# Performance work log

Hardware: AMD Instinct MI355X
Metric: run time of the kernel (lower is better)

Reference implementation:

```python
import jax, jax.numpy as jnp
import numpy as np

N = 40000
K = 16
NUM_CLASSES = 8
BN_EPS = 1e-5


def _mlp(h, W1, b1, g, bt, m, v, W2, b2):
    # Linear -> ReLU -> BatchNorm1d (eval mode, running stats) -> Linear
    h = jax.nn.relu(h @ W1 + b1)
    h = (h - m) / jnp.sqrt(v + BN_EPS) * g + bt
    return h @ W2 + b2


def _normals(pos, nbr):
    # cross product of first two neighbor offsets, normalized; fallback [0,0,1]
    v1 = pos[nbr[:, 0]] - pos
    v2 = pos[nbr[:, 1]] - pos
    n = jnp.cross(v1, v2)
    nrm = jnp.linalg.norm(n, axis=-1, keepdims=True)
    unit = n / jnp.maximum(nrm, 1e-12)
    up = jnp.array([0.0, 0.0, 1.0], dtype=pos.dtype)
    return jnp.where(nrm > 0, unit, up)


def _pointnet_conv(x, pos, nbr_all, W1, b1, g, bt, m, v, W2, b2):
    # PyG PointNetConv: msg = local_nn(cat[x_j, pos_j - pos_i]); max-aggregate
    xj = x[nbr_all]                        # [N, K+1, F]
    rel = pos[nbr_all] - pos[:, None, :]   # [N, K+1, 3]
    msg = _mlp(jnp.concatenate([xj, rel], axis=-1), W1, b1, g, bt, m, v, W2, b2)
    return msg.max(axis=1)


def setup_inputs():
    key = jax.random.key(0)
    ks = jax.random.split(key, 32)

    def lin_w(k, fi, fo):
        return (jax.random.normal(k, (fi, fo), jnp.float32) / np.sqrt(fi)).astype(jnp.float32)

    def vec(k, d, scale=0.01):
        return scale * jax.random.normal(k, (d,), jnp.float32)

    return {
        "pos": jax.random.normal(ks[0], (N, 3), jnp.float32),
        "neighbor_idx": jax.random.randint(ks[1], (N, K), 0, N),
        # local_features: Linear(9,64), ReLU, BN(64), Linear(64,128)
        "W1": lin_w(ks[2], 9, 64), "b1": vec(ks[3], 64),
        "g1": 1.0 + 0.1 * jax.random.normal(ks[4], (64,), jnp.float32),
        "bt1": vec(ks[5], 64), "m1": vec(ks[6], 64, 0.1),
        "v1": jax.random.uniform(ks[7], (64,), jnp.float32, minval=0.5, maxval=1.5),
        "W2": lin_w(ks[8], 64, 128), "b2": vec(ks[9], 128),
        # roof_features: Linear(131,128), ReLU, BN(128), Linear(128,256)
        "W3": lin_w(ks[10], 131, 128), "b3": vec(ks[11], 128),
        "g2": 1.0 + 0.1 * jax.random.normal(ks[12], (128,), jnp.float32),
        "bt2": vec(ks[13], 128), "m2": vec(ks[14], 128, 0.1),
        "v2": jax.random.uniform(ks[15], (128,), jnp.float32, minval=0.5, maxval=1.5),
        "W4": lin_w(ks[16], 128, 256), "b4": vec(ks[17], 256),
        # classifier: Linear(256, num_classes)
        "Wc": lin_w(ks[18], 256, NUM_CLASSES), "bc": vec(ks[19], NUM_CLASSES),
    }


def reference(pos, neighbor_idx, W1, b1, g1, bt1, m1, v1, W2, b2,
              W3, b3, g2, bt2, m2, v2, W4, b4, Wc, bc):
    x = pos  # data.x is used as both features and coordinates
    normals = _normals(pos, neighbor_idx)
    x = jnp.concatenate([x, normals], axis=1)  # [N, 6]
    # PointNetConv adds self-loops by default
    self_idx = jnp.arange(pos.shape[0], dtype=neighbor_idx.dtype)[:, None]
    nbr_all = jnp.concatenate([neighbor_idx, self_idx], axis=1)  # [N, K+1]
    x = jax.nn.relu(_pointnet_conv(x, pos, nbr_all, W1, b1, g1, bt1, m1, v1, W2, b2))
    x = jax.nn.relu(_pointnet_conv(x, pos, nbr_all, W3, b3, g2, bt2, m2, v2, W4, b4))
    logits = x @ Wc + bc
    return jax.nn.log_softmax(logits, axis=-1)
```

## Files before the change

kernel.cpp:

```cpp
#include <hip/hip_runtime.h>
#include <math.h>

#define NPTS 40000
#define KNBR 16
#define BN_EPS 1e-5f

typedef __attribute__((ext_vector_type(8))) short v8s;
typedef __attribute__((ext_vector_type(4))) float f32x4;

__device__ __forceinline__ unsigned short f2bf(float f) {
    union { float f; unsigned int u; } c; c.f = f;
    unsigned int u = c.u + 0x7fffu + ((c.u >> 16) & 1u);
    return (unsigned short)(u >> 16);
}
__device__ __forceinline__ float bflo(unsigned int u) {
    union { unsigned int u; float f; } c; c.u = u << 16; return c.f;
}
__device__ __forceinline__ float bfhi(unsigned int u) {
    union { unsigned int u; float f; } c; c.u = u & 0xffff0000u; return c.f;
}

__global__ __launch_bounds__(256, 4)
void k1_b1(const float* __restrict__ pos, const int* __restrict__ nbr,
           const float* __restrict__ W1, const float* __restrict__ b1,
           unsigned short* __restrict__ B1) {
    int p = blockIdx.x * 4 + (threadIdx.x >> 6);
    int k = threadIdx.x & 63;
    float px = pos[p * 3 + 0], py = pos[p * 3 + 1], pz = pos[p * 3 + 2];
    int n0 = nbr[p * KNBR + 0], n1 = nbr[p * KNBR + 1];
    float ax = pos[n0 * 3 + 0] - px, ay = pos[n0 * 3 + 1] - py, az = pos[n0 * 3 + 2] - pz;
    float bx = pos[n1 * 3 + 0] - px, by = pos[n1 * 3 + 1] - py, bz = pos[n1 * 3 + 2] - pz;
    float cx = ay * bz - az * by;
    float cy = az * bx - ax * bz;
    float cz = ax * by - ay * bx;
    float nrm = sqrtf(cx * cx + cy * cy + cz * cz);
    float inv = 1.0f / fmaxf(nrm, 1e-12f);
    float ux, uy, uz;
    if (nrm > 0.0f) { ux = cx * inv; uy = cy * inv; uz = cz * inv; }
    else            { ux = 0.0f;     uy = 0.0f;     uz = 1.0f;     }
    float acc = b1[k];
    acc = fmaf(px, W1[0 * 64 + k], acc);
    acc = fmaf(py, W1[1 * 64 + k], acc);
    acc = fmaf(pz, W1[2 * 64 + k], acc);
    acc = fmaf(ux, W1[3 * 64 + k], acc);
    acc = fmaf(uy, W1[4 * 64 + k], acc);
    acc = fmaf(uz, W1[5 * 64 + k], acc);
    B1[p * 64 + k] = f2bf(acc);
}

#define PTS2 32
__global__ __launch_bounds__(256, 2)
void k2_conv1_mfma(const float* __restrict__ pos, const int* __restrict__ nbr,
                   const unsigned short* __restrict__ B1, const float* __restrict__ W1,
                   const float* __restrict__ g1, const float* __restrict__ bt1,
                   const float* __restrict__ m1, const float* __restrict__ v1,
                   const float* __restrict__ W2, const float* __restrict__ b2,
                   const float* __restrict__ W3, const float* __restrict__ b3,
                   unsigned short* __restrict__ A2) {
    __shared__ __align__(16) unsigned char Tl[2][16 * 128];
    __shared__ __align__(16) unsigned char Hl[32 * 256];
    __shared__ float Ssf1[32 * 128];

    const int tid  = threadIdx.x;
    const int wv   = tid >> 6;
    const int lane = tid & 63;
    const int lgrp = lane >> 4;
    const int lmod = lane & 15;

    v8s Bf2[2][2];
    float b2c[2];
#pragma unroll
    for (int nt = 0; nt < 2; ++nt) {
        const int col = wv * 32 + nt * 16 + lmod;
        b2c[nt] = b2[col];
#pragma unroll
        for (int kt = 0; kt < 2; ++kt)
#pragma unroll
            for (int j = 0; j < 8; ++j)
                Bf2[nt][kt][j] = (short)f2bf(W2[(kt * 32 + lgrp * 8 + j) * 128 + col]);
    }
    const int ch0 = (lane & 31) * 2;
    const int rsub = lane >> 5;
    const float w6a = W1[6 * 64 + ch0],     w7a = W1[7 * 64 + ch0],     w8a = W1[8 * 64 + ch0];
    const float w6b = W1[6 * 64 + ch0 + 1], w7b = W1[7 * 64 + ch0 + 1], w8b = W1[8 * 64 + ch0 + 1];
    const float s1a = g1[ch0] * rsqrtf(v1[ch0] + BN_EPS);
    const float o1a = bt1[ch0] - m1[ch0] * s1a;
    const float s1b = g1[ch0 + 1] * rsqrtf(v1[ch0 + 1] + BN_EPS);
    const float o1b = bt1[ch0 + 1] - m1[ch0 + 1] * s1b;

    const int base = blockIdx.x * PTS2;

#pragma unroll
    for (int pr = 0; pr < 16; ++pr) {
        const int pl = pr * 2 + rsub;
        const unsigned int a = *(const unsigned int*)&B1[(size_t)(base + pl) * 64 + ch0];
        const float ta = fmaf(fmaxf(bflo(a), 0.f), s1a, o1a);
        const float tb = fmaf(fmaxf(bfhi(a), 0.f), s1b, o1b);
        const unsigned int w = (unsigned int)f2bf(ta) | ((unsigned int)f2bf(tb) << 16);
        const int row = pl & 15;
        int byte = row * 128 + ch0 * 2;
        byte ^= (row & 7) << 4;
        *(unsigned int*)(Tl[pl >> 4] + byte) = w;
    }
    __syncthreads();
    {
        f32x4 accS[2][2];
#pragma unroll
        for (int hf = 0; hf < 2; ++hf)
#pragma unroll
            for (int nt = 0; nt < 2; ++nt) accS[hf][nt] = f32x4{0.f, 0.f, 0.f, 0.f};
#pragma unroll
        for (int hf = 0; hf < 2; ++hf)
#pragma unroll
            for (int kt = 0; kt < 2; ++kt) {
                int b0 = lmod * 128 + kt * 64 + lgrp * 16;
                b0 ^= (lmod & 7) << 4;
                const v8s a0 = *(const v8s*)(Tl[hf] + b0);
#pragma unroll
                for (int nt = 0; nt < 2; ++nt)
                    accS[hf][nt] = __builtin_amdgcn_mfma_f32_16x16x32_bf16(a0, Bf2[nt][kt], accS[hf][nt], 0, 0, 0);
            }
#pragma unroll
        for (int hf = 0; hf < 2; ++hf)
#pragma unroll
            for (int nt = 0; nt < 2; ++nt)
#pragma unroll
                for (int reg = 0; reg < 4; ++reg)
                    Ssf1[(hf * 16 + lgrp * 4 + reg) * 128 + wv * 32 + nt * 16 + lmod] = accS[hf][nt][reg];
    }
    __syncthreads();

    {
        const int i = base;
        const float cx = pos[i * 3 + 0], cy = pos[i * 3 + 1], cz = pos[i * 3 + 2];
#pragma unroll
        for (int it = 0; it < 2; ++it) {
            const int m = it * 8 + wv * 2 + rsub;
            const int idx = nbr[i * KNBR + m];
            const unsigned int a = *(const unsigned int*)&B1[(size_t)idx * 64 + ch0];
            const float rx = pos[idx * 3 + 0] - cx;
            const float ry = pos[idx * 3 + 1] - cy;
            const float rz = pos[idx * 3 + 2] - cz;
            float pa = bflo(a);
            pa = fmaf(rx, w6a, pa); pa = fmaf(ry, w7a, pa); pa = fmaf(rz, w8a, pa);
            float pb = bfhi(a);
            pb = fmaf(rx, w6b, pb); pb = fmaf(ry, w7b, pb); pb = fmaf(rz, w8b, pb);
            const float ta = fmaf(fmaxf(pa, 0.f), s1a, o1a);
            const float tb = fmaf(fmaxf(pb, 0.f), s1b, o1b);
            const unsigned int w = (unsigned int)f2bf(ta) | ((unsigned int)f2bf(tb) << 16);
            int byte = m * 128 + ch0 * 2;
            byte ^= (m & 7) << 4;
            *(unsigned int*)(Tl[0] + byte) = w;
        }
    }
    unsigned int aCur[2], aNxt[2];
    float pCx[2], pCy[2], pCz[2], pNx[2], pNy[2], pNz[2];
#pragma unroll
    for (int it = 0; it < 2; ++it) { aCur[it] = 0u; aNxt[it] = 0u; pCx[it]=pCy[it]=pCz[it]=pNx[it]=pNy[it]=pNz[it]=0.f; }
    {
        const int in_ = base + 1;
#pragma unroll
        for (int it = 0; it < 2; ++it) {
            const int m = it * 8 + wv * 2 + rsub;
            const int idx = nbr[in_ * KNBR + m];
            aCur[it] = *(const unsigned int*)&B1[(size_t)idx * 64 + ch0];
            pCx[it] = pos[idx * 3 + 0]; pCy[it] = pos[idx * 3 + 1]; pCz[it] = pos[idx * 3 + 2];
        }
    }
    __syncthreads();

    for (int p = 0; p < PTS2; ++p) {
        const int buf = p & 1;
        if (p < PTS2 - 2) {
            const int in2 = base + p + 2;
#pragma unroll
            for (int it = 0; it < 2; ++it) {
                const int m = it * 8 + wv * 2 + rsub;
                const int idx = nbr[in2 * KNBR + m];
                aNxt[it] = *(const unsigned int*)&B1[(size_t)idx * 64 + ch0];
                pNx[it] = pos[idx * 3 + 0]; pNy[it] = pos[idx * 3 + 1]; pNz[it] = pos[idx * 3 + 2];
            }
        }
        f32x4 acc0[2];
        acc0[0] = f32x4{0.f, 0.f, 0.f, 0.f};
        acc0[1] = f32x4{0.f, 0.f, 0.f, 0.f};
#pragma unroll
        for (int kt = 0; kt < 2; ++kt) {
            int b0 = lmod * 128 + kt * 64 + lgrp * 16;
            b0 ^= (lmod & 7) << 4;
            const v8s a0 = *(const v8s*)(Tl[buf] + b0);
#pragma unroll
            for (int nt = 0; nt < 2; ++nt)
                acc0[nt] = __builtin_amdgcn_mfma_f32_16x16x32_bf16(a0, Bf2[nt][kt], acc0[nt], 0, 0, 0);
        }
#pragma unroll
        for (int nt = 0; nt < 2; ++nt) {
            float mv = fmaxf(fmaxf(acc0[nt][0], acc0[nt][1]),
                             fmaxf(acc0[nt][2], acc0[nt][3]));
            mv = fmaxf(mv, __shfl_xor(mv, 16));
            mv = fmaxf(mv, __shfl_xor(mv, 32));
            const float ss = Ssf1[p * 128 + wv * 32 + nt * 16 + lmod];
            const float h = fmaxf(fmaxf(mv, ss) + b2c[nt], 0.f);
            if (lgrp == 0) {
                int hb = p * 256 + (wv * 32 + nt * 16 + lmod) * 2;
                hb ^= (p & 7) << 4;
                *(unsigned short*)(Hl + hb) = f2bf(h);
            }
        }
        if (p < PTS2 - 1) {
            const int in_ = base + p + 1;
            const float ccx = pos[in_ * 3 + 0], ccy = pos[in_ * 3 + 1], ccz = pos[in_ * 3 + 2];
#pragma unroll
            for (int it = 0; it < 2; ++it) {
                const int m = it * 8 + wv * 2 + rsub;
                const float rx = pCx[it] - ccx, ry = pCy[it] - ccy, rz = pCz[it] - ccz;
                float pa = bflo(aCur[it]);
                pa = fmaf(rx, w6a, pa); pa = fmaf(ry, w7a, pa); pa = fmaf(rz, w8a, pa);
                float pb = bfhi(aCur[it]);
                pb = fmaf(rx, w6b, pb); pb = fmaf(ry, w7b, pb); pb = fmaf(rz, w8b, pb);
                const float ta = fmaf(fmaxf(pa, 0.f), s1a, o1a);
                const float tb = fmaf(fmaxf(pb, 0.f), s1b, o1b);
                const unsigned int w = (unsigned int)f2bf(ta) | ((unsigned int)f2bf(tb) << 16);
                int byte = m * 128 + ch0 * 2;
                byte ^= (m & 7) << 4;
                *(unsigned int*)(Tl[buf ^ 1] + byte) = w;
            }
        }
        __syncthreads();
#pragma unroll
        for (int it = 0; it < 2; ++it) {
            aCur[it] = aNxt[it];
            pCx[it] = pNx[it]; pCy[it] = pNy[it]; pCz[it] = pNz[it];
        }
    }

    v8s Wf3[2][4];
    float b3c[2];
#pragma unroll
    for (int nt = 0; nt < 2; ++nt) {
        const int col = wv * 32 + nt * 16 + lmod;
        b3c[nt] = b3[col];
#pragma unroll
        for (int kt = 0; kt < 4; ++kt)
#pragma unroll
            for (int j = 0; j < 8; ++j)
                Wf3[nt][kt][j] = (short)f2bf(W3[(kt * 32 + lgrp * 8 + j) * 128 + col]);
    }
    f32x4 accA[2][2];
#pragma unroll
    for (int mt = 0; mt < 2; ++mt)
#pragma unroll
        for (int nt = 0; nt < 2; ++nt) accA[mt][nt] = f32x4{0.f, 0.f, 0.f, 0.f};
#pragma unroll
    for (int kt = 0; kt < 4; ++kt) {
#pragma unroll
        for (int mt = 0; mt < 2; ++mt) {
            int ba = (mt * 16 + lmod) * 256 + kt * 64 + lgrp * 16;
            ba ^= (lmod & 7) << 4;
            const v8s aH = *(const v8s*)(Hl + ba);
#pragma unroll
            for (int nt = 0; nt < 2; ++nt)
                accA[mt][nt] = __builtin_amdgcn_mfma_f32_16x16x32_bf16(aH, Wf3[nt][kt], accA[mt][nt], 0, 0, 0);
        }
    }
#pragma unroll
    for (int mt = 0; mt < 2; ++mt)
#pragma unroll
        for (int nt = 0; nt < 2; ++nt)
#pragma unroll
            for (int reg = 0; reg < 4; ++reg) {
                const int row = base + mt * 16 + lgrp * 4 + reg;
                const int col = wv * 32 + nt * 16 + lmod;
                A2[(size_t)row * 128 + col] = f2bf(accA[mt][nt][reg] + b3c[nt]);
            }
}

#define PTS4 32
__global__ __launch_bounds__(256, 2)
void k4_conv2_mfma(const float* __restrict__ pos, const int* __restrict__ nbr,
                   const unsigned short* __restrict__ A2, const float* __restrict__ W3,
                   const float* __restrict__ g2, const float* __restrict__ bt2,
                   const float* __restrict__ m2, const float* __restrict__ v2,
                   const float* __restrict__ W4, const float* __restrict__ b4,
                   const float* __restrict__ Wc,
                   float* __restrict__ Z) {
    __shared__ __align__(16) unsigned char Tl[2][16 * 256];
    __shared__ float Ssf[32 * 256];

    const int tid  = threadIdx.x;
    const int wv   = tid >> 6;
    const int lane = tid & 63;
    const int lgrp = lane >> 4;
    const int lmod = lane & 15;

    v8s Bf[4][4];
#pragma unroll
    for (int nt = 0; nt < 4; ++nt) {
        const int col = wv * 64 + nt * 16 + lmod;
#pragma unroll
        for (int kt = 0; kt < 4; ++kt)
#pragma unroll
            for (int j = 0; j < 8; ++j)
                Bf[nt][kt][j] = (short)f2bf(W4[(kt * 32 + lgrp * 8 + j) * 256 + col]);
    }
    float wcls[4][8]; float b4c[4];
#pragma unroll
    for (int nt = 0; nt < 4; ++nt) {
        const int col = wv * 64 + nt * 16 + lmod;
        b4c[nt] = b4[col];
#pragma unroll
        for (int c = 0; c < 8; ++c) wcls[nt][c] = Wc[col * 8 + c];
    }
    const int ch0 = lane * 2;
    const float bw0a = W3[128 * 128 + ch0],     bw1a = W3[129 * 128 + ch0],     bw2a = W3[130 * 128 + ch0];
    const float bw0b = W3[128 * 128 + ch0 + 1], bw1b = W3[129 * 128 + ch0 + 1], bw2b = W3[130 * 128 + ch0 + 1];
    const float sa = g2[ch0] * rsqrtf(v2[ch0] + BN_EPS);
    const float oa = bt2[ch0] - m2[ch0] * sa;
    const float sb = g2[ch0 + 1] * rsqrtf(v2[ch0 + 1] + BN_EPS);
    const float ob = bt2[ch0 + 1] - m2[ch0 + 1] * sb;

    const int base = blockIdx.x * PTS4;

#pragma unroll
    for (int pl = 0; pl < 16; ++pl) {
        {
            const unsigned int a = *(const unsigned int*)&A2[(size_t)(base + pl) * 128 + ch0];
            const float ta = fmaf(fmaxf(bflo(a), 0.f), sa, oa);
            const float tb = fmaf(fmaxf(bfhi(a), 0.f), sb, ob);
            const unsigned int w = (unsigned int)f2bf(ta) | ((unsigned int)f2bf(tb) << 16);
            int byte = pl * 256 + ch0 * 2;
            byte ^= (pl & 7) << 4;
            *(unsigned int*)(Tl[0] + byte) = w;
        }
        {
            const unsigned int a = *(const unsigned int*)&A2[(size_t)(base + 16 + pl) * 128 + ch0];
            const float ta = fmaf(fmaxf(bflo(a), 0.f), sa, oa);
            const float tb = fmaf(fmaxf(bfhi(a), 0.f), sb, ob);
            const unsigned int w = (unsigned int)f2bf(ta) | ((unsigned int)f2bf(tb) << 16);
            int byte = pl * 256 + ch0 * 2;
            byte ^= (pl & 7) << 4;
            *(unsigned int*)(Tl[1] + byte) = w;
        }
    }
    __syncthreads();
    {
        f32x4 accS[2][4];
#pragma unroll
        for (int hf = 0; hf < 2; ++hf)
#pragma unroll
            for (int nt = 0; nt < 4; ++nt) accS[hf][nt] = f32x4{0.f, 0.f, 0.f, 0.f};
#pragma unroll
        for (int hf = 0; hf < 2; ++hf)
#pragma unroll
            for (int kt = 0; kt < 4; ++kt) {
                int b0 = lmod * 256 + kt * 64 + lgrp * 16;
                b0 ^= (lmod & 7) << 4;
                const v8s a0 = *(const v8s*)(Tl[hf] + b0);
#pragma unroll
                for (int nt = 0; nt < 4; ++nt)
                    accS[hf][nt] = __builtin_amdgcn_mfma_f32_16x16x32_bf16(a0, Bf[nt][kt], accS[hf][nt], 0, 0, 0);
            }
#pragma unroll
        for (int hf = 0; hf < 2; ++hf)
#pragma unroll
            for (int nt = 0; nt < 4; ++nt)
#pragma unroll
                for (int reg = 0; reg < 4; ++reg)
                    Ssf[(hf * 16 + lgrp * 4 + reg) * 256 + wv * 64 + nt * 16 + lmod] = accS[hf][nt][reg];
    }
    __syncthreads();

    {
        const int i = base;
        const float cx = pos[i * 3 + 0], cy = pos[i * 3 + 1], cz = pos[i * 3 + 2];
#pragma unroll
        for (int it = 0; it < 4; ++it) {
            const int m = it * 4 + wv;
            const int idx = nbr[i * KNBR + m];
            const unsigned int a = *(const unsigned int*)&A2[(size_t)idx * 128 + ch0];
            const float rx = pos[idx * 3 + 0] - cx;
            const float ry = pos[idx * 3 + 1] - cy;
            const float rz = pos[idx * 3 + 2] - cz;
            float pa = bflo(a);
            pa = fmaf(rx, bw0a, pa); pa = fmaf(ry, bw1a, pa); pa = fmaf(rz, bw2a, pa);
            float pb = bfhi(a);
            pb = fmaf(rx, bw0b, pb); pb = fmaf(ry, bw1b, pb); pb = fmaf(rz, bw2b, pb);
            const float ta = fmaf(fmaxf(pa, 0.f), sa, oa);
            const float tb = fmaf(fmaxf(pb, 0.f), sb, ob);
            const unsigned int w = (unsigned int)f2bf(ta) | ((unsigned int)f2bf(tb) << 16);
            int byte = m * 256 + ch0 * 2;
            byte ^= (m & 7) << 4;
            *(unsigned int*)(Tl[0] + byte) = w;
        }
    }
    unsigned int aCur[4], aNxt[4];
    float pCx[4], pCy[4], pCz[4], pNx[4], pNy[4], pNz[4];
#pragma unroll
    for (int it = 0; it < 4; ++it) { aCur[it] = 0u; aNxt[it] = 0u; pCx[it]=pCy[it]=pCz[it]=pNx[it]=pNy[it]=pNz[it]=0.f; }
    {
        const int in_ = base + 1;
#pragma unroll
        for (int it = 0; it < 4; ++it) {
            const int m = it * 4 + wv;
            const int idx = nbr[in_ * KNBR + m];
            aCur[it] = *(const unsigned int*)&A2[(size_t)idx * 128 + ch0];
            pCx[it] = pos[idx * 3 + 0]; pCy[it] = pos[idx * 3 + 1]; pCz[it] = pos[idx * 3 + 2];
        }
    }
    __syncthreads();

    for (int p = 0; p < PTS4; ++p) {
        const int buf = p & 1;
        if (p < PTS4 - 2) {
            const int in2 = base + p + 2;
#pragma unroll
            for (int it = 0; it < 4; ++it) {
                const int m = it * 4 + wv;
                const int idx = nbr[in2 * KNBR + m];
                aNxt[it] = *(const unsigned int*)&A2[(size_t)idx * 128 + ch0];
                pNx[it] = pos[idx * 3 + 0]; pNy[it] = pos[idx * 3 + 1]; pNz[it] = pos[idx * 3 + 2];
            }
        }
        f32x4 acc0[4];
#pragma unroll
        for (int nt = 0; nt < 4; ++nt) acc0[nt] = f32x4{0.f, 0.f, 0.f, 0.f};
#pragma unroll
        for (int kt = 0; kt < 4; ++kt) {
            int b0 = lmod * 256 + kt * 64 + lgrp * 16;
            b0 ^= (lmod & 7) << 4;
            const v8s a0 = *(const v8s*)(Tl[buf] + b0);
#pragma unroll
            for (int nt = 0; nt < 4; ++nt)
                acc0[nt] = __builtin_amdgcn_mfma_f32_16x16x32_bf16(a0, Bf[nt][kt], acc0[nt], 0, 0, 0);
        }
        float part[8];
#pragma unroll
        for (int c = 0; c < 8; ++c) part[c] = 0.f;
#pragma unroll
        for (int nt = 0; nt < 4; ++nt) {
            float mv = fmaxf(fmaxf(acc0[nt][0], acc0[nt][1]),
                             fmaxf(acc0[nt][2], acc0[nt][3]));
            mv = fmaxf(mv, __shfl_xor(mv, 16));
            mv = fmaxf(mv, __shfl_xor(mv, 32));
            const float ss = Ssf[p * 256 + wv * 64 + nt * 16 + lmod];
            const float h = fmaxf(fmaxf(mv, ss) + b4c[nt], 0.f);
#pragma unroll
            for (int c = 0; c < 8; ++c) part[c] = fmaf(h, wcls[nt][c], part[c]);
        }
#pragma unroll
        for (int c = 0; c < 8; ++c) {
            part[c] += __shfl_xor(part[c], 1);
            part[c] += __shfl_xor(part[c], 2);
            part[c] += __shfl_xor(part[c], 4);
            part[c] += __shfl_xor(part[c], 8);
        }
        if (lane == 0) {
#pragma unroll
            for (int c = 0; c < 8; ++c)
                Z[(size_t)(base + p) * 32 + wv * 8 + c] = part[c];
        }
        if (p < PTS4 - 1) {
            const int in_ = base + p + 1;
            const float ccx = pos[in_ * 3 + 0], ccy = pos[in_ * 3 + 1], ccz = pos[in_ * 3 + 2];
#pragma unroll
            for (int it = 0; it < 4; ++it) {
                const int m = it * 4 + wv;
                const float rx = pCx[it] - ccx, ry = pCy[it] - ccy, rz = pCz[it] - ccz;
                float pa = bflo(aCur[it]);
                pa = fmaf(rx, bw0a, pa); pa = fmaf(ry, bw1a, pa); pa = fmaf(rz, bw2a, pa);
                float pb = bfhi(aCur[it]);
                pb = fmaf(rx, bw0b, pb); pb = fmaf(ry, bw1b, pb); pb = fmaf(rz, bw2b, pb);
                const float ta = fmaf(fmaxf(pa, 0.f), sa, oa);
                const float tb = fmaf(fmaxf(pb, 0.f), sb, ob);
                const unsigned int w = (unsigned int)f2bf(ta) | ((unsigned int)f2bf(tb) << 16);
                int byte = m * 256 + ch0 * 2;
                byte ^= (m & 7) << 4;
                *(unsigned int*)(Tl[buf ^ 1] + byte) = w;
            }
        }
        __syncthreads();
#pragma unroll
        for (int it = 0; it < 4; ++it) {
            aCur[it] = aNxt[it];
            pCx[it] = pNx[it]; pCy[it] = pNy[it]; pCz[it] = pNz[it];
        }
    }
}

__global__ __launch_bounds__(256, 4)
void k5_softmax(const float* __restrict__ Z, const float* __restrict__ bc,
                float* __restrict__ out) {
    const int i = blockIdx.x * 256 + threadIdx.x;
    if (i >= NPTS) return;
    float z[8];
#pragma unroll
    for (int c = 0; c < 8; ++c) z[c] = bc[c];
#pragma unroll
    for (int w = 0; w < 4; ++w) {
        const float4 a = *(const float4*)&Z[(size_t)i * 32 + w * 8 + 0];
        const float4 b = *(const float4*)&Z[(size_t)i * 32 + w * 8 + 4];
        z[0] += a.x; z[1] += a.y; z[2] += a.z; z[3] += a.w;
        z[4] += b.x; z[5] += b.y; z[6] += b.z; z[7] += b.w;
    }
    float mz = z[0];
#pragma unroll
    for (int c = 1; c < 8; ++c) mz = fmaxf(mz, z[c]);
    float se = 0.f;
#pragma unroll
    for (int c = 0; c < 8; ++c) se += expf(z[c] - mz);
    const float lse = mz + logf(se);
#pragma unroll
    for (int c = 0; c < 8; ++c) out[(size_t)i * 8 + c] = z[c] - lse;
}

extern "C" void kernel_launch(void* const* d_in, const int* in_sizes, int n_in,
                              void* d_out, int out_size, void* d_ws, size_t ws_size,
                              hipStream_t stream) {
    const float* pos = (const float*)d_in[0];
    const int*   nbr = (const int*)d_in[1];
    const float* W1  = (const float*)d_in[2];
    const float* b1  = (const float*)d_in[3];
    const float* g1  = (const float*)d_in[4];
    const float* bt1 = (const float*)d_in[5];
    const float* m1  = (const float*)d_in[6];
    const float* v1  = (const float*)d_in[7];
    const float* W2  = (const float*)d_in[8];
    const float* b2  = (const float*)d_in[9];
    const float* W3  = (const float*)d_in[10];
    const float* b3  = (const float*)d_in[11];
    const float* g2  = (const float*)d_in[12];
    const float* bt2 = (const float*)d_in[13];
    const float* m2  = (const float*)d_in[14];
    const float* v2  = (const float*)d_in[15];
    const float* W4  = (const float*)d_in[16];
    const float* b4  = (const float*)d_in[17];
    const float* Wc  = (const float*)d_in[18];
    const float* bc  = (const float*)d_in[19];
    float* out = (float*)d_out;

    unsigned short* B1 = (unsigned short*)d_ws;
    unsigned short* A2 = B1 + (size_t)NPTS * 64;
    float* Z = (float*)(A2 + (size_t)NPTS * 128);

    k1_b1<<<NPTS / 4, 256, 0, stream>>>(pos, nbr, W1, b1, B1);
    k2_conv1_mfma<<<NPTS / PTS2, 256, 0, stream>>>(pos, nbr, B1, W1, g1, bt1, m1, v1,
                                                   W2, b2, W3, b3, A2);
    k4_conv2_mfma<<<NPTS / PTS4, 256, 0, stream>>>(pos, nbr, A2, W3, g2, bt2, m2, v2,
                                                   W4, b4, Wc, Z);
    k5_softmax<<<(NPTS + 255) / 256, 256, 0, stream>>>(Z, bc, out);
}
```

Before: 320.9 us.

## Process four points per pipeline step with one wave per point gather

Both conv kernels now handle a group of four points per loop iteration, with each wave gathering all 16 neighbors of one point using a wave-uniform (readfirstlane) index. This replaces the old one-point-per-iteration loop, so there are a quarter as many barriers and each gather load is larger. The self-term scratch is stored as bf16 instead of fp32 to fit the larger 64-row tiles in LDS, and in conv2 the classifier weights are read from memory per use instead of being held in registers. In exchange, the kernels use more LDS and more registers for prefetch, and the bf16 self-term adds some rounding error.

Measured after the change: 319.8 us. Within noise of the previous version (-0.3%).

```diff
diff --git a/kernel.cpp b/kernel.cpp
--- a/kernel.cpp
+++ b/kernel.cpp
@@ -18,6 +18,9 @@
 }
 __device__ __forceinline__ float bfhi(unsigned int u) {
     union { unsigned int u; float f; } c; c.u = u & 0xffff0000u; return c.f;
+}
+__device__ __forceinline__ float bf2f(unsigned short u) {
+    union { unsigned int u; float f; } c; c.u = ((unsigned int)u) << 16; return c.f;
 }
 
 __global__ __launch_bounds__(256, 4)
@@ -49,6 +52,7 @@
 }
 
 #define PTS2 32
+#define NG2 8
 __global__ __launch_bounds__(256, 2)
 void k2_conv1_mfma(const float* __restrict__ pos, const int* __restrict__ nbr,
                    const unsigned short* __restrict__ B1, const float* __restrict__ W1,
@@ -57,9 +61,9 @@
                    const float* __restrict__ W2, const float* __restrict__ b2,
                    const float* __restrict__ W3, const float* __restrict__ b3,
                    unsigned short* __restrict__ A2) {
-    __shared__ __align__(16) unsigned char Tl[2][16 * 128];
+    __shared__ __align__(16) unsigned char Tl[2][64 * 128];
     __shared__ __align__(16) unsigned char Hl[32 * 256];
-    __shared__ float Ssf1[32 * 128];
+    __shared__ unsigned short Ssb[32 * 128];
 
     const int tid  = threadIdx.x;
     const int wv   = tid >> 6;
@@ -79,28 +83,21 @@
             for (int j = 0; j < 8; ++j)
                 Bf2[nt][kt][j] = (short)f2bf(W2[(kt * 32 + lgrp * 8 + j) * 128 + col]);
     }
-    const int ch0 = (lane & 31) * 2;
-    const int rsub = lane >> 5;
-    const float w6a = W1[6 * 64 + ch0],     w7a = W1[7 * 64 + ch0],     w8a = W1[8 * 64 + ch0];
-    const float w6b = W1[6 * 64 + ch0 + 1], w7b = W1[7 * 64 + ch0 + 1], w8b = W1[8 * 64 + ch0 + 1];
-    const float s1a = g1[ch0] * rsqrtf(v1[ch0] + BN_EPS);
-    const float o1a = bt1[ch0] - m1[ch0] * s1a;
-    const float s1b = g1[ch0 + 1] * rsqrtf(v1[ch0 + 1] + BN_EPS);
-    const float o1b = bt1[ch0 + 1] - m1[ch0 + 1] * s1b;
+    const int ch = lane;
+    const float w6 = W1[6 * 64 + ch], w7 = W1[7 * 64 + ch], w8 = W1[8 * 64 + ch];
+    const float s1 = g1[ch] * rsqrtf(v1[ch] + BN_EPS);
+    const float o1 = bt1[ch] - m1[ch] * s1;
 
     const int base = blockIdx.x * PTS2;
 
 #pragma unroll
-    for (int pr = 0; pr < 16; ++pr) {
-        const int pl = pr * 2 + rsub;
-        const unsigned int a = *(const unsigned int*)&B1[(size_t)(base + pl) * 64 + ch0];
-        const float ta = fmaf(fmaxf(bflo(a), 0.f), s1a, o1a);
-        const float tb = fmaf(fmaxf(bfhi(a), 0.f), s1b, o1b);
-        const unsigned int w = (unsigned int)f2bf(ta) | ((unsigned int)f2bf(tb) << 16);
-        const int row = pl & 15;
-        int byte = row * 128 + ch0 * 2;
-        byte ^= (row & 7) << 4;
-        *(unsigned int*)(Tl[pl >> 4] + byte) = w;
+    for (int r = 0; r < 8; ++r) {
+        const int pl = wv * 8 + r;
+        const float bv = bf2f(B1[(size_t)(base + pl) * 64 + ch]);
+        const float t = fmaf(fmaxf(bv, 0.f), s1, o1);
+        int byte = pl * 128 + ch * 2;
+        byte ^= (pl & 7) << 4;
+        *(unsigned short*)(Tl[0] + byte) = f2bf(t);
     }
     __syncthreads();
     {
@@ -113,9 +110,10 @@
         for (int hf = 0; hf < 2; ++hf)
 #pragma unroll
             for (int kt = 0; kt < 2; ++kt) {
-                int b0 = lmod * 128 + kt * 64 + lgrp * 16;
-                b0 ^= (lmod & 7) << 4;
-                const v8s a0 = *(const v8s*)(Tl[hf] + b0);
+                const int row = hf * 16 + lmod;
+                int b0 = row * 128 + kt * 64 + lgrp * 16;
+                b0 ^= (row & 7) << 4;
+                const v8s a0 = *(const v8s*)(Tl[0] + b0);
 #pragma unroll
                 for (int nt = 0; nt < 2; ++nt)
                     accS[hf][nt] = __builtin_amdgcn_mfma_f32_16x16x32_bf16(a0, Bf2[nt][kt], accS[hf][nt], 0, 0, 0);
@@ -126,112 +124,97 @@
             for (int nt = 0; nt < 2; ++nt)
 #pragma unroll
                 for (int reg = 0; reg < 4; ++reg)
-                    Ssf1[(hf * 16 + lgrp * 4 + reg) * 128 + wv * 32 + nt * 16 + lmod] = accS[hf][nt][reg];
+                    Ssb[(hf * 16 + lgrp * 4 + reg) * 128 + wv * 32 + nt * 16 + lmod] =
+                        f2bf(accS[hf][nt][reg]);
     }
     __syncthreads();
 
     {
-        const int i = base;
-        const float cx = pos[i * 3 + 0], cy = pos[i * 3 + 1], cz = pos[i * 3 + 2];
-#pragma unroll
-        for (int it = 0; it < 2; ++it) {
-            const int m = it * 8 + wv * 2 + rsub;
-            const int idx = nbr[i * KNBR + m];
-            const unsigned int a = *(const unsigned int*)&B1[(size_t)idx * 64 + ch0];
+        const int i0 = base + wv;
+        const float cx = pos[i0 * 3 + 0], cy = pos[i0 * 3 + 1], cz = pos[i0 * 3 + 2];
+#pragma unroll
+        for (int m = 0; m < 16; ++m) {
+            int idx = nbr[i0 * KNBR + m];
+            idx = __builtin_amdgcn_readfirstlane(idx);
+            const float bv = bf2f(B1[(size_t)idx * 64 + ch]);
             const float rx = pos[idx * 3 + 0] - cx;
             const float ry = pos[idx * 3 + 1] - cy;
             const float rz = pos[idx * 3 + 2] - cz;
-            float pa = bflo(a);
-            pa = fmaf(rx, w6a, pa); pa = fmaf(ry, w7a, pa); pa = fmaf(rz, w8a, pa);
-            float pb = bfhi(a);
-            pb = fmaf(rx, w6b, pb); pb = fmaf(ry, w7b, pb); pb = fmaf(rz, w8b, pb);
-            const float ta = fmaf(fmaxf(pa, 0.f), s1a, o1a);
-            const float tb = fmaf(fmaxf(pb, 0.f), s1b, o1b);
-            const unsigned int w = (unsigned int)f2bf(ta) | ((unsigned int)f2bf(tb) << 16);
-            int byte = m * 128 + ch0 * 2;
-            byte ^= (m & 7) << 4;
-            *(unsigned int*)(Tl[0] + byte) = w;
-        }
-    }
-    unsigned int aCur[2], aNxt[2];
-    float pCx[2], pCy[2], pCz[2], pNx[2], pNy[2], pNz[2];
-#pragma unroll
-    for (int it = 0; it < 2; ++it) { aCur[it] = 0u; aNxt[it] = 0u; pCx[it]=pCy[it]=pCz[it]=pNx[it]=pNy[it]=pNz[it]=0.f; }
-    {
-        const int in_ = base + 1;
-#pragma unroll
-        for (int it = 0; it < 2; ++it) {
-            const int m = it * 8 + wv * 2 + rsub;
-            const int idx = nbr[in_ * KNBR + m];
-            aCur[it] = *(const unsigned int*)&B1[(size_t)idx * 64 + ch0];
-            pCx[it] = pos[idx * 3 + 0]; pCy[it] = pos[idx * 3 + 1]; pCz[it] = pos[idx * 3 + 2];
+            float pre = bv;
+            pre = fmaf(rx, w6, pre); pre = fmaf(ry, w7, pre); pre = fmaf(rz, w8, pre);
+            const float t = fmaf(fmaxf(pre, 0.f), s1, o1);
+            const int row = wv * 16 + m;
+            int byte = row * 128 + ch * 2;
+            byte ^= (row & 7) << 4;
+            *(unsigned short*)(Tl[0] + byte) = f2bf(t);
         }
     }
     __syncthreads();
 
-    for (int p = 0; p < PTS2; ++p) {
-        const int buf = p & 1;
-        if (p < PTS2 - 2) {
-            const int in2 = base + p + 2;
-#pragma unroll
-            for (int it = 0; it < 2; ++it) {
-                const int m = it * 8 + wv * 2 + rsub;
-                const int idx = nbr[in2 * KNBR + m];
-                aNxt[it] = *(const unsigned int*)&B1[(size_t)idx * 64 + ch0];
-                pNx[it] = pos[idx * 3 + 0]; pNy[it] = pos[idx * 3 + 1]; pNz[it] = pos[idx * 3 + 2];
-            }
-        }
-        f32x4 acc0[2];
-        acc0[0] = f32x4{0.f, 0.f, 0.f, 0.f};
-        acc0[1] = f32x4{0.f, 0.f, 0.f, 0.f};
-#pragma unroll
-        for (int kt = 0; kt < 2; ++kt) {
-            int b0 = lmod * 128 + kt * 64 + lgrp * 16;
-            b0 ^= (lmod & 7) << 4;
-            const v8s a0 = *(const v8s*)(Tl[buf] + b0);
-#pragma unroll
-            for (int nt = 0; nt < 2; ++nt)
-                acc0[nt] = __builtin_amdgcn_mfma_f32_16x16x32_bf16(a0, Bf2[nt][kt], acc0[nt], 0, 0, 0);
-        }
-#pragma unroll
-        for (int nt = 0; nt < 2; ++nt) {
-            float mv = fmaxf(fmaxf(acc0[nt][0], acc0[nt][1]),
-                             fmaxf(acc0[nt][2], acc0[nt][3]));
-            mv = fmaxf(mv, __shfl_xor(mv, 16));
-            mv = fmaxf(mv, __shfl_xor(mv, 32));
-            const float ss = Ssf1[p * 128 + wv * 32 + nt * 16 + lmod];
-            const float h = fmaxf(fmaxf(mv, ss) + b2c[nt], 0.f);
-            if (lgrp == 0) {
-                int hb = p * 256 + (wv * 32 + nt * 16 + lmod) * 2;
-                hb ^= (p & 7) << 4;
-                *(unsigned short*)(Hl + hb) = f2bf(h);
-            }
-        }
-        if (p < PTS2 - 1) {
-            const int in_ = base + p + 1;
-            const float ccx = pos[in_ * 3 + 0], ccy = pos[in_ * 3 + 1], ccz = pos[in_ * 3 + 2];
-#pragma unroll
-            for (int it = 0; it < 2; ++it) {
-                const int m = it * 8 + wv * 2 + rsub;
-                const float rx = pCx[it] - ccx, ry = pCy[it] - ccy, rz = pCz[it] - ccz;
-                float pa = bflo(aCur[it]);
-                pa = fmaf(rx, w6a, pa); pa = fmaf(ry, w7a, pa); pa = fmaf(rz, w8a, pa);
-                float pb = bfhi(aCur[it]);
-                pb = fmaf(rx, w6b, pb); pb = fmaf(ry, w7b, pb); pb = fmaf(rz, w8b, pb);
-                const float ta = fmaf(fmaxf(pa, 0.f), s1a, o1a);
-                const float tb = fmaf(fmaxf(pb, 0.f), s1b, o1b);
-                const unsigned int w = (unsigned int)f2bf(ta) | ((unsigned int)f2bf(tb) << 16);
-                int byte = m * 128 + ch0 * 2;
-                byte ^= (m & 7) << 4;
-                *(unsigned int*)(Tl[buf ^ 1] + byte) = w;
+    unsigned short aN[16];
+    int idxN[16];
+    float cNx = 0.f, cNy = 0.f, cNz = 0.f;
+    for (int g = 0; g < NG2; ++g) {
+        const int buf = g & 1;
+        if (g < NG2 - 1) {
+            const int iN = base + (g + 1) * 4 + wv;
+            cNx = pos[iN * 3 + 0]; cNy = pos[iN * 3 + 1]; cNz = pos[iN * 3 + 2];
+#pragma unroll
+            for (int m = 0; m < 16; ++m) {
+                int idx = nbr[iN * KNBR + m];
+                idx = __builtin_amdgcn_readfirstlane(idx);
+                idxN[m] = idx;
+                aN[m] = B1[(size_t)idx * 64 + ch];
+            }
+        }
+#pragma unroll
+        for (int rb = 0; rb < 4; ++rb) {
+            f32x4 acc[2];
+            acc[0] = f32x4{0.f, 0.f, 0.f, 0.f};
+            acc[1] = f32x4{0.f, 0.f, 0.f, 0.f};
+#pragma unroll
+            for (int kt = 0; kt < 2; ++kt) {
+                const int row = rb * 16 + lmod;
+                int b0 = row * 128 + kt * 64 + lgrp * 16;
+                b0 ^= (row & 7) << 4;
+                const v8s a0 = *(const v8s*)(Tl[buf] + b0);
+#pragma unroll
+                for (int nt = 0; nt < 2; ++nt)
+                    acc[nt] = __builtin_amdgcn_mfma_f32_16x16x32_bf16(a0, Bf2[nt][kt], acc[nt], 0, 0, 0);
+            }
+            const int pl = g * 4 + rb;
+#pragma unroll
+            for (int nt = 0; nt < 2; ++nt) {
+                float mv = fmaxf(fmaxf(acc[nt][0], acc[nt][1]),
+                                 fmaxf(acc[nt][2], acc[nt][3]));
+                mv = fmaxf(mv, __shfl_xor(mv, 16));
+                mv = fmaxf(mv, __shfl_xor(mv, 32));
+                const float ss = bf2f(Ssb[pl * 128 + wv * 32 + nt * 16 + lmod]);
+                const float h = fmaxf(fmaxf(mv, ss) + b2c[nt], 0.f);
+                if (lgrp == 0) {
+                    int hb = pl * 256 + (wv * 32 + nt * 16 + lmod) * 2;
+                    hb ^= (pl & 7) << 4;
+                    *(unsigned short*)(Hl + hb) = f2bf(h);
+                }
+            }
+        }
+        if (g < NG2 - 1) {
+#pragma unroll
+            for (int m = 0; m < 16; ++m) {
+                const int idx = idxN[m];
+                const float rx = pos[idx * 3 + 0] - cNx;
+                const float ry = pos[idx * 3 + 1] - cNy;
+                const float rz = pos[idx * 3 + 2] - cNz;
+                float pre = bf2f(aN[m]);
+                pre = fmaf(rx, w6, pre); pre = fmaf(ry, w7, pre); pre = fmaf(rz, w8, pre);
+                const float t = fmaf(fmaxf(pre, 0.f), s1, o1);
+                const int row = wv * 16 + m;
+                int byte = row * 128 + ch * 2;
+                byte ^= (row & 7) << 4;
+                *(unsigned short*)(Tl[buf ^ 1] + byte) = f2bf(t);
             }
         }
         __syncthreads();
-#pragma unroll
-        for (int it = 0; it < 2; ++it) {
-            aCur[it] = aNxt[it];
-            pCx[it] = pNx[it]; pCy[it] = pNy[it]; pCz[it] = pNz[it];
-        }
     }
 
     v8s Wf3[2][4];
@@ -276,6 +259,7 @@
 }
 
 #define PTS4 32
+#define NG4 8
 __global__ __launch_bounds__(256, 2)
 void k4_conv2_mfma(const float* __restrict__ pos, const int* __restrict__ nbr,
                    const unsigned short* __restrict__ A2, const float* __restrict__ W3,
@@ -284,8 +268,8 @@
                    const float* __restrict__ W4, const float* __restrict__ b4,
                    const float* __restrict__ Wc,
                    float* __restrict__ Z) {
-    __shared__ __align__(16) unsigned char Tl[2][16 * 256];
-    __shared__ float Ssf[32 * 256];
+    __shared__ __align__(16) unsigned char Tl[2][64 * 256];
+    __shared__ unsigned short Ssb[32 * 256];
 
     const int tid  = threadIdx.x;
     const int wv   = tid >> 6;
@@ -303,14 +287,9 @@
             for (int j = 0; j < 8; ++j)
                 Bf[nt][kt][j] = (short)f2bf(W4[(kt * 32 + lgrp * 8 + j) * 256 + col]);
     }
-    float wcls[4][8]; float b4c[4];
-#pragma unroll
-    for (int nt = 0; nt < 4; ++nt) {
-        const int col = wv * 64 + nt * 16 + lmod;
-        b4c[nt] = b4[col];
-#pragma unroll
-        for (int c = 0; c < 8; ++c) wcls[nt][c] = Wc[col * 8 + c];
-    }
+    float b4c[4];
+#pragma unroll
+    for (int nt = 0; nt < 4; ++nt) b4c[nt] = b4[wv * 64 + nt * 16 + lmod];
     const int ch0 = lane * 2;
     const float bw0a = W3[128 * 128 + ch0],     bw1a = W3[129 * 128 + ch0],     bw2a = W3[130 * 128 + ch0];
     const float bw0b = W3[128 * 128 + ch0 + 1], bw1b = W3[129 * 128 + ch0 + 1], bw2b = W3[130 * 128 + ch0 + 1];
@@ -322,25 +301,15 @@
     const int base = blockIdx.x * PTS4;
 
 #pragma unroll
-    for (int pl = 0; pl < 16; ++pl) {
-        {
-            const unsigned int a = *(const unsigned int*)&A2[(size_t)(base + pl) * 128 + ch0];
-            const float ta = fmaf(fmaxf(bflo(a), 0.f), sa, oa);
-            const float tb = fmaf(fmaxf(bfhi(a), 0.f), sb, ob);
-            const unsigned int w = (unsigned int)f2bf(ta) | ((unsigned int)f2bf(tb) << 16);
-            int byte = pl * 256 + ch0 * 2;
-            byte ^= (pl & 7) << 4;
-            *(unsigned int*)(Tl[0] + byte) = w;
-        }
-        {
-            const unsigned int a = *(const unsigned int*)&A2[(size_t)(base + 16 + pl) * 128 + ch0];
-            const float ta = fmaf(fmaxf(bflo(a), 0.f), sa, oa);
-            const float tb = fmaf(fmaxf(bfhi(a), 0.f), sb, ob);
-            const unsigned int w = (unsigned int)f2bf(ta) | ((unsigned int)f2bf(tb) << 16);
-            int byte = pl * 256 + ch0 * 2;
-            byte ^= (pl & 7) << 4;
-            *(unsigned int*)(Tl[1] + byte) = w;
-        }
+    for (int r = 0; r < 8; ++r) {
+        const int pl = wv * 8 + r;
+        const unsigned int a = *(const unsigned int*)&A2[(size_t)(base + pl) * 128 + ch0];
+        const float ta = fmaf(fmaxf(bflo(a), 0.f), sa, oa);
+        const float tb = fmaf(fmaxf(bfhi(a), 0.f), sb, ob);
+        const unsigned int w = (unsigned int)f2bf(ta) | ((unsigned int)f2bf(tb) << 16);
+        int byte = pl * 256 + ch0 * 2;
+        byte ^= (pl & 7) << 4;
+        *(unsigned int*)(Tl[0] + byte) = w;
     }
     __syncthreads();
     {
@@ -353,9 +322,10 @@
         for (int hf = 0; hf < 2; ++hf)
 #pragma unroll
             for (int kt = 0; kt < 4; ++kt) {
-                int b0 = lmod * 256 + kt * 64 + lgrp * 16;
-                b0 ^= (lmod & 7) << 4;
-                const v8s a0 = *(const v8s*)(Tl[hf] + b0);
+                const int row = hf * 16 + lmod;
+                int b0 = row * 256 + kt * 64 + lgrp * 16;
+                b0 ^= (row & 7) << 4;
+                const v8s a0 = *(const v8s*)(Tl[0] + b0);
 #pragma unroll
                 for (int nt = 0; nt < 4; ++nt)
                     accS[hf][nt] = __builtin_amdgcn_mfma_f32_16x16x32_bf16(a0, Bf[nt][kt], accS[hf][nt], 0, 0, 0);
@@ -366,17 +336,18 @@
             for (int nt = 0; nt < 4; ++nt)
 #pragma unroll
                 for (int reg = 0; reg < 4; ++reg)
-                    Ssf[(hf * 16 + lgrp * 4 + reg) * 256 + wv * 64 + nt * 16 + lmod] = accS[hf][nt][reg];
+                    Ssb[(hf * 16 + lgrp * 4 + reg) * 256 + wv * 64 + nt * 16 + lmod] =
+                        f2bf(accS[hf][nt][reg]);
     }
     __syncthreads();
 
     {
-        const int i = base;
-        const float cx = pos[i * 3 + 0], cy = pos[i * 3 + 1], cz = pos[i * 3 + 2];
-#pragma unroll
-        for (int it = 0; it < 4; ++it) {
-            const int m = it * 4 + wv;
-            const int idx = nbr[i * KNBR + m];
+        const int i0 = base + wv;
+        const float cx = pos[i0 * 3 + 0], cy = pos[i0 * 3 + 1], cz = pos[i0 * 3 + 2];
+#pragma unroll
+        for (int m = 0; m < 16; ++m) {
+            int idx = nbr[i0 * KNBR + m];
+            idx = __builtin_amdgcn_readfirstlane(idx);
             const unsigned int a = *(const unsigned int*)&A2[(size_t)idx * 128 + ch0];
             const float rx = pos[idx * 3 + 0] - cx;
             const float ry = pos[idx * 3 + 1] - cy;
@@ -388,102 +359,99 @@
             const float ta = fmaf(fmaxf(pa, 0.f), sa, oa);
             const float tb = fmaf(fmaxf(pb, 0.f), sb, ob);
             const unsigned int w = (unsigned int)f2bf(ta) | ((unsigned int)f2bf(tb) << 16);
-            int byte = m * 256 + ch0 * 2;
-            byte ^= (m & 7) << 4;
+            const int row = wv * 16 + m;
+            int byte = row * 256 + ch0 * 2;
+            byte ^= (row & 7) << 4;
             *(unsigned int*)(Tl[0] + byte) = w;
         }
     }
-    unsigned int aCur[4], aNxt[4];
-    float pCx[4], pCy[4], pCz[4], pNx[4], pNy[4], pNz[4];
-#pragma unroll
-    for (int it = 0; it < 4; ++it) { aCur[it] = 0u; aNxt[it] = 0u; pCx[it]=pCy[it]=pCz[it]=pNx[it]=pNy[it]=pNz[it]=0.f; }
-    {
-        const int in_ = base + 1;
-#pragma unroll
-        for (int it = 0; it < 4; ++it) {
-            const int m = it * 4 + wv;
-            const int idx = nbr[in_ * KNBR + m];
-            aCur[it] = *(const unsigned int*)&A2[(size_t)idx * 128 + ch0];
-            pCx[it] = pos[idx * 3 + 0]; pCy[it] = pos[idx * 3 + 1]; pCz[it] = pos[idx * 3 + 2];
-        }
-    }
     __syncthreads();
 
-    for (int p = 0; p < PTS4; ++p) {
-        const int buf = p & 1;
-        if (p < PTS4 - 2) {
-            const int in2 = base + p + 2;
-#pragma unroll
-            for (int it = 0; it < 4; ++it) {
-                const int m = it * 4 + wv;
-                const int idx = nbr[in2 * KNBR + m];
-                aNxt[it] = *(const unsigned int*)&A2[(size_t)idx * 128 + ch0];
-                pNx[it] = pos[idx * 3 + 0]; pNy[it] = pos[idx * 3 + 1]; pNz[it] = pos[idx * 3 + 2];
-            }
-        }
-        f32x4 acc0[4];
-#pragma unroll
-        for (int nt = 0; nt < 4; ++nt) acc0[nt] = f32x4{0.f, 0.f, 0.f, 0.f};
-#pragma unroll
-        for (int kt = 0; kt < 4; ++kt) {
-            int b0 = lmod * 256 + kt * 64 + lgrp * 16;
-            b0 ^= (lmod & 7) << 4;
-            const v8s a0 = *(const v8s*)(Tl[buf] + b0);
-#pragma unroll
-            for (int nt = 0; nt < 4; ++nt)
-                acc0[nt] = __builtin_amdgcn_mfma_f32_16x16x32_bf16(a0, Bf[nt][kt], acc0[nt], 0, 0, 0);
-        }
-        float part[8];
-#pragma unroll
-        for (int c = 0; c < 8; ++c) part[c] = 0.f;
-#pragma unroll
-        for (int nt = 0; nt < 4; ++nt) {
-            float mv = fmaxf(fmaxf(acc0[nt][0], acc0[nt][1]),
-                             fmaxf(acc0[nt][2], acc0[nt][3]));
-            mv = fmaxf(mv, __shfl_xor(mv, 16));
-            mv = fmaxf(mv, __shfl_xor(mv, 32));
-            const float ss = Ssf[p * 256 + wv * 64 + nt * 16 + lmod];
-            const float h = fmaxf(fmaxf(mv, ss) + b4c[nt], 0.f);
-#pragma unroll
-            for (int c = 0; c < 8; ++c) part[c] = fmaf(h, wcls[nt][c], part[c]);
-        }
-#pragma unroll
-        for (int c = 0; c < 8; ++c) {
-            part[c] += __shfl_xor(part[c], 1);
-            part[c] += __shfl_xor(part[c], 2);
-            part[c] += __shfl_xor(part[c], 4);
-            part[c] += __shfl_xor(part[c], 8);
-        }
-        if (lane == 0) {
-#pragma unroll
-            for (int c = 0; c < 8; ++c)
-                Z[(size_t)(base + p) * 32 + wv * 8 + c] = part[c];
-        }
-        if (p < PTS4 - 1) {
-            const int in_ = base + p + 1;
-            const float ccx = pos[in_ * 3 + 0], ccy = pos[in_ * 3 + 1], ccz = pos[in_ * 3 + 2];
-#pragma unroll
-            for (int it = 0; it < 4; ++it) {
-                const int m = it * 4 + wv;
-                const float rx = pCx[it] - ccx, ry = pCy[it] - ccy, rz = pCz[it] - ccz;
-                float pa = bflo(aCur[it]);
+    unsigned int aN[16];
+    int idxN[16];
+    float cNx = 0.f, cNy = 0.f, cNz = 0.f;
+    for (int g = 0; g < NG4; ++g) {
+        const int buf = g & 1;
+        if (g < NG4 - 1) {
+            const int iN = base + (g + 1) * 4 + wv;
+            cNx = pos[iN * 3 + 0]; cNy = pos[iN * 3 + 1]; cNz = pos[iN * 3 + 2];
+#pragma unroll
+            for (int m = 0; m < 16; ++m) {
+                int idx = nbr[iN * KNBR + m];
+                idx = __builtin_amdgcn_readfirstlane(idx);
+                idxN[m] = idx;
+                aN[m] = *(const unsigned int*)&A2[(size_t)idx * 128 + ch0];
+            }
+        }
+#pragma unroll
+        for (int rb = 0; rb < 4; ++rb) {
+            f32x4 acc[4];
+#pragma unroll
+            for (int nt = 0; nt < 4; ++nt) acc[nt] = f32x4{0.f, 0.f, 0.f, 0.f};
+#pragma unroll
+            for (int kt = 0; kt < 4; ++kt) {
+                const int row = rb * 16 + lmod;
+                int b0 = row * 256 + kt * 64 + lgrp * 16;
+                b0 ^= (row & 7) << 4;
+                const v8s a0 = *(const v8s*)(Tl[buf] + b0);
+#pragma unroll
+                for (int nt = 0; nt < 4; ++nt)
+                    acc[nt] = __builtin_amdgcn_mfma_f32_16x16x32_bf16(a0, Bf[nt][kt], acc[nt], 0, 0, 0);
+            }
+            const int pl = g * 4 + rb;
+            float part[8];
+#pragma unroll
+            for (int c = 0; c < 8; ++c) part[c] = 0.f;
+#pragma unroll
+            for (int nt = 0; nt < 4; ++nt) {
+                float mv = fmaxf(fmaxf(acc[nt][0], acc[nt][1]),
+                                 fmaxf(acc[nt][2], acc[nt][3]));
+                mv = fmaxf(mv, __shfl_xor(mv, 16));
+                mv = fmaxf(mv, __shfl_xor(mv, 32));
+                const float ss = bf2f(Ssb[pl * 256 + wv * 64 + nt * 16 + lmod]);
+                const float h = fmaxf(fmaxf(mv, ss) + b4c[nt], 0.f);
+                const int col = wv * 64 + nt * 16 + lmod;
+                const float4 wc0 = *(const float4*)&Wc[col * 8 + 0];
+                const float4 wc1 = *(const float4*)&Wc[col * 8 + 4];
+                part[0] = fmaf(h, wc0.x, part[0]); part[1] = fmaf(h, wc0.y, part[1]);
+                part[2] = fmaf(h, wc0.z, part[2]); part[3] = fmaf(h, wc0.w, part[3]);
+                part[4] = fmaf(h, wc1.x, part[4]); part[5] = fmaf(h, wc1.y, part[5]);
+                part[6] = fmaf(h, wc1.z, part[6]); part[7] = fmaf(h, wc1.w, part[7]);
+            }
+#pragma unroll
+            for (int c = 0; c < 8; ++c) {
+                part[c] += __shfl_xor(part[c], 1);
+                part[c] += __shfl_xor(part[c], 2);
+                part[c] += __shfl_xor(part[c], 4);
+                part[c] += __shfl_xor(part[c], 8);
+            }
+            if (lane == 0) {
+#pragma unroll
+                for (int c = 0; c < 8; ++c)
+                    Z[(size_t)(base + pl) * 32 + wv * 8 + c] = part[c];
+            }
+        }
+        if (g < NG4 - 1) {
+#pragma unroll
+            for (int m = 0; m < 16; ++m) {
+                const int idx = idxN[m];
+                const float rx = pos[idx * 3 + 0] - cNx;
+                const float ry = pos[idx * 3 + 1] - cNy;
+                const float rz = pos[idx * 3 + 2] - cNz;
+                float pa = bflo(aN[m]);
                 pa = fmaf(rx, bw0a, pa); pa = fmaf(ry, bw1a, pa); pa = fmaf(rz, bw2a, pa);
-                float pb = bfhi(aCur[it]);
+                float pb = bfhi(aN[m]);
                 pb = fmaf(rx, bw0b, pb); pb = fmaf(ry, bw1b, pb); pb = fmaf(rz, bw2b, pb);
                 const float ta = fmaf(fmaxf(pa, 0.f), sa, oa);
                 const float tb = fmaf(fmaxf(pb, 0.f), sb, ob);
                 const unsigned int w = (unsigned int)f2bf(ta) | ((unsigned int)f2bf(tb) << 16);
-                int byte = m * 256 + ch0 * 2;
-                byte ^= (m & 7) << 4;
+                const int row = wv * 16 + m;
+                int byte = row * 256 + ch0 * 2;
+                byte ^= (row & 7) << 4;
                 *(unsigned int*)(Tl[buf ^ 1] + byte) = w;
             }
         }
         __syncthreads();
-#pragma unroll
-        for (int it = 0; it < 4; ++it) {
-            aCur[it] = aNxt[it];
-            pCx[it] = pNx[it]; pCy[it] = pNy[it]; pCz[it] = pNz[it];
-        }
     }
 }
 
```
